# Performance work log

Hardware: AMD Instinct MI355X
Metric: run time of the kernel (lower is better)

## Reference

```python
import jax, jax.numpy as jnp
import numpy as np

DIM = 192; HEADS = 6; HDIM = DIM // HEADS
WS = (2, 8, 8); SS = (1, 4, 4)
B, D, H, W = 2, 8, 64, 64
N = WS[0] * WS[1] * WS[2]          # 128 tokens per window
MLP_H = int(DIM * 2.0)
SCALE = HDIM ** -0.5


def _rel_pos_index_np():
    wd, wh, ww = WS
    coords = np.stack(np.meshgrid(np.arange(wd), np.arange(wh), np.arange(ww), indexing='ij'))
    cf = coords.reshape(3, -1)                      # (3, N)
    rel = (cf[:, :, None] - cf[:, None, :]).transpose(1, 2, 0)  # (N, N, 3)
    rel[..., 0] += wd - 1; rel[..., 1] += wh - 1; rel[..., 2] += ww - 1
    rel[..., 0] *= (2 * wh - 1) * (2 * ww - 1)
    rel[..., 1] *= (2 * ww - 1)
    return rel.sum(-1).astype(np.int32)            # (N, N)


def _compute_mask_np():
    wd, wh, ww = WS; sd, sh, sw = SS
    Dp = -(-D // wd) * wd; Hp = -(-H // wh) * wh; Wp = -(-W // ww) * ww
    img = np.zeros((1, Dp, Hp, Wp, 1), np.float32)
    cnt = 0
    for ds in (slice(0, -wd), slice(-wd, -sd), slice(-sd, None)):
        for hs in (slice(0, -wh), slice(-wh, -sh), slice(-sh, None)):
            for vs in (slice(0, -ww), slice(-ww, -sw), slice(-sw, None)):
                img[:, ds, hs, vs, :] = cnt; cnt += 1
    m = img.reshape(1, Dp // wd, wd, Hp // wh, wh, Wp // ww, ww, 1)
    m = m.transpose(0, 1, 3, 5, 2, 4, 6, 7).reshape(-1, N)       # (nW, N)
    am = m[:, None, :] - m[:, :, None]
    return np.where(am != 0, -100.0, 0.0).astype(np.float32)     # (nW, N, N)


def setup_inputs() -> dict:
    key = jax.random.key(0)
    ks = jax.random.split(key, 6)
    f = lambda k, s: (jax.random.normal(k, s, jnp.float32) * 0.02)
    n_bias = (2 * WS[0] - 1) * (2 * WS[1] - 1) * (2 * WS[2] - 1)  # 675
    return dict(
        x=jax.random.normal(ks[0], (B, D, H, W, DIM), jnp.float32),
        mask_matrix=jnp.asarray(_compute_mask_np()),
        rel_pos_index=jnp.asarray(_rel_pos_index_np()),
        gamma1=jnp.ones((DIM,), jnp.float32), beta1=jnp.zeros((DIM,), jnp.float32),
        w_qkv=f(ks[1], (3 * DIM, DIM)), b_qkv=jnp.zeros((3 * DIM,), jnp.float32),
        rpb=f(ks[2], (n_bias, HEADS)),
        w_proj=f(ks[3], (DIM, DIM)), b_proj=jnp.zeros((DIM,), jnp.float32),
        gamma2=jnp.ones((DIM,), jnp.float32), beta2=jnp.zeros((DIM,), jnp.float32),
        w_fc1=f(ks[4], (MLP_H, DIM)), b_fc1=jnp.zeros((MLP_H,), jnp.float32),
        w_fc2=f(ks[5], (DIM, MLP_H)), b_fc2=jnp.zeros((DIM,), jnp.float32),
    )


def _ln(x, g, b, eps=1e-5):
    mu = x.mean(-1, keepdims=True)
    var = ((x - mu) ** 2).mean(-1, keepdims=True)
    return (x - mu) * jax.lax.rsqrt(var + eps) * g + b


def _stl(x, mask, rpi, gamma1, beta1, w_qkv, b_qkv, rpb, w_proj, b_proj,
         gamma2, beta2, w_fc1, b_fc1, w_fc2, b_fc2):
    wd, wh, ww = WS; sd, sh, sw = SS
    # ---- part1: LN -> pad -> roll -> window attention -> reverse ----
    xn = _ln(x, gamma1, beta1)
    pd = (wd - D % wd) % wd; ph = (wh - H % wh) % wh; pw = (ww - W % ww) % ww
    xn = jnp.pad(xn, ((0, 0), (0, pd), (0, ph), (0, pw), (0, 0)))
    Dp, Hp, Wp = D + pd, H + ph, W + pw
    sx = jnp.roll(xn, (-sd, -sh, -sw), axis=(1, 2, 3))
    # window partition -> (Bw, N, C)
    xw = sx.reshape(B, Dp // wd, wd, Hp // wh, wh, Wp // ww, ww, DIM)
    xw = xw.transpose(0, 1, 3, 5, 2, 4, 6, 7).reshape(-1, N, DIM)
    Bw = xw.shape[0]
    qkv = (xw @ w_qkv.T + b_qkv).reshape(Bw, N, 3, HEADS, HDIM).transpose(2, 0, 3, 1, 4)
    q, k, v = qkv[0] * SCALE, qkv[1], qkv[2]
    attn = jnp.einsum('bhnd,bhmd->bhnm', q, k)
    bias = rpb[rpi.reshape(-1)].reshape(N, N, HEADS).transpose(2, 0, 1)  # (H, N, N)
    attn = attn + bias[None]
    nW = mask.shape[0]
    attn = (attn.reshape(Bw // nW, nW, HEADS, N, N) + mask[None, :, None]).reshape(Bw, HEADS, N, N)
    attn = jax.nn.softmax(attn, axis=-1)
    out = jnp.einsum('bhnm,bhmd->bhnd', attn, v).transpose(0, 2, 1, 3).reshape(Bw, N, DIM)
    out = out @ w_proj.T + b_proj
    # window reverse -> un-roll -> slice
    sx = out.reshape(B, Dp // wd, Hp // wh, Wp // ww, wd, wh, ww, DIM)
    sx = sx.transpose(0, 1, 4, 2, 5, 3, 6, 7).reshape(B, Dp, Hp, Wp, DIM)
    part1 = jnp.roll(sx, (sd, sh, sw), axis=(1, 2, 3))[:, :D, :H, :W, :]
    x = x + part1
    # ---- part2: LN -> MLP (GELU, exact) ----
    y = _ln(x, gamma2, beta2)
    h = jax.nn.gelu(y @ w_fc1.T + b_fc1, approximate=False)
    return x + (h @ w_fc2.T + b_fc2)


def reference(x, mask_matrix, rel_pos_index, gamma1, beta1, w_qkv, b_qkv, rpb,
              w_proj, b_proj, gamma2, beta2, w_fc1, b_fc1, w_fc2, b_fc2):
    return _stl(x, mask_matrix, rel_pos_index, gamma1, beta1, w_qkv, b_qkv, rpb,
                w_proj, b_proj, gamma2, beta2, w_fc1, b_fc1, w_fc2, b_fc2)
```

## Files before the change

kernel.cpp:

```cpp
#include <hip/hip_runtime.h>
#include <hip/hip_bf16.h>
#include <math.h>

#define TOKS   65536
#define DIMC   192
#define NTOK   128
#define MLPH   384
#define QSCALE 0.17677669529663687f

typedef unsigned short u16;
typedef unsigned int   u32;
typedef __attribute__((ext_vector_type(8))) short bf16x8;
typedef __attribute__((ext_vector_type(4))) float f32x4;

static __device__ __forceinline__ float gelu_exact(float v) {
    return 0.5f * v * (1.f + erff(v * 0.70710678118654752f));
}
static __device__ __forceinline__ u16 f2bf(float f) {
    __hip_bfloat16 h = __float2bfloat16(f);
    return *reinterpret_cast<u16*>(&h);
}
static __device__ __forceinline__ float bf2f(u16 b) {
    u32 u = ((u32)b) << 16;
    float f;
    __builtin_memcpy(&f, &u, 4);
    return f;
}
static __device__ __forceinline__ void gl_lds16(const u16* g, u16* l) {
    __builtin_amdgcn_global_load_lds(
        (const __attribute__((address_space(1))) void*)g,
        (__attribute__((address_space(3))) void*)l, 16, 0, 0);
}

#define OFF_XW   0u
#define OFF_Q    6291456u
#define OFF_K    12582912u
#define OFF_V    18874368u
#define OFF_BF   25165824u
#define OFF_WB   25264128u

__global__ __launch_bounds__(256) void k_cvt(const float* __restrict__ a,
                                             const float* __restrict__ b,
                                             const float* __restrict__ c,
                                             const float* __restrict__ d,
                                             u16* __restrict__ o) {
    int i = blockIdx.x * 256 + threadIdx.x;
    float v;
    if (i < 110592) v = a[i];
    else if (i < 147456) v = b[i - 110592];
    else if (i < 221184) v = c[i - 147456];
    else v = d[i - 221184];
    o[i] = f2bf(v);
}

__global__ __launch_bounds__(256) void k_bias(const float* __restrict__ rpb,
                                              const int* __restrict__ rpi,
                                              u16* __restrict__ biasw) {
    int idx = blockIdx.x * 256 + threadIdx.x;
    int h = idx >> 14;
    int n = (idx >> 7) & 127;
    int slot = idx & 127;
    int m = ((slot & 7) << 4) + (slot >> 3);
    biasw[idx] = f2bf(rpb[rpi[n * 128 + m] * 6 + h]);
}

template<bool PERMUTE>
__global__ __launch_bounds__(256) void k_ln(const float* __restrict__ x,
                                            const float* __restrict__ gamma,
                                            const float* __restrict__ beta,
                                            u16* __restrict__ out) {
    int tid  = threadIdx.x;
    int lane = tid & 63, wv = tid >> 6;
    int tk = blockIdx.x * 4 + wv;
    size_t src;
    if (PERMUTE) {
        int w_all = tk >> 7, t = tk & 127;
        int b  = w_all >> 8, rem = w_all & 255;
        int di = rem >> 6, hi = (rem >> 3) & 7, wi = rem & 7;
        int qd = (di * 2 + (t >> 6) + 1) & 7;
        int qh = (hi * 8 + ((t >> 3) & 7) + 4) & 63;
        int qw = (wi * 8 + (t & 7) + 4) & 63;
        src = ((size_t)(((b * 8 + qd) * 64 + qh) * 64 + qw)) * DIMC;
    } else {
        src = (size_t)tk * DIMC;
    }
    float v0 = x[src + lane];
    float v1 = x[src + 64 + lane];
    float v2 = x[src + 128 + lane];
    float s  = v0 + v1 + v2;
    float sq = v0 * v0 + v1 * v1 + v2 * v2;
    #pragma unroll
    for (int off = 32; off; off >>= 1) {
        s  += __shfl_xor(s, off);
        sq += __shfl_xor(sq, off);
    }
    float mu   = s * (1.f / 192.f);
    float var  = sq * (1.f / 192.f) - mu * mu;
    float rstd = rsqrtf(var + 1e-5f);
    size_t o = (size_t)tk * DIMC;
    out[o + lane]       = f2bf((v0 - mu) * rstd * gamma[lane]       + beta[lane]);
    out[o + 64 + lane]  = f2bf((v1 - mu) * rstd * gamma[64 + lane]  + beta[64 + lane]);
    out[o + 128 + lane] = f2bf((v2 - mu) * rstd * gamma[128 + lane] + beta[128 + lane]);
}

template<int MODE, int KD>
__global__ __launch_bounds__(256) void k_mgemm(const u16* __restrict__ A,
                                               const u16* __restrict__ W,
                                               const float* __restrict__ bias,
                                               void* __restrict__ outp,
                                               const float* __restrict__ aux,
                                               u16* __restrict__ q_o,
                                               u16* __restrict__ k_o,
                                               u16* __restrict__ v_o) {
    __shared__ u16 As[2][128 * 64];
    u16*   Eu = (u16*)As;
    float* Ef = (float*)As;
    const int tid = threadIdx.x;
    const int wv = tid >> 6, l = tid & 63;
    const int l15 = l & 15, g4 = l >> 4;
    const int wm = wv >> 1, wn = wv & 1;
    const size_t m0 = (size_t)blockIdx.x * 128;
    const int n0 = blockIdx.y * 64;
    const int srow = l >> 3, scol = l & 7;

    f32x4 acc[4][2] = {};

    auto STAGE = [&](int b, int t) {
        const u16* Ab = A + m0 * KD + t * 64;
        #pragma unroll
        for (int j = 0; j < 4; ++j) {
            int row = (wv * 4 + j) * 8 + srow;
            int sc  = scol ^ (row & 7);
            gl_lds16(Ab + (size_t)row * KD + sc * 8, &As[b][(wv * 4 + j) * 512]);
        }
    };
    auto COMPUTE = [&](int b, int t) {
        #pragma unroll
        for (int kk = 0; kk < 2; ++kk) {
            bf16x8 bfr[2];
            #pragma unroll
            for (int nt = 0; nt < 2; ++nt)
                bfr[nt] = *(const bf16x8*)&W[(size_t)(n0 + wn * 32 + nt * 16 + l15) * KD
                                             + t * 64 + kk * 32 + g4 * 8];
            #pragma unroll
            for (int mt = 0; mt < 4; ++mt) {
                int row  = wm * 64 + mt * 16 + l15;
                int slot = (kk * 4 + g4) ^ (row & 7);
                bf16x8 afr = *(const bf16x8*)&As[b][row * 64 + slot * 8];
                #pragma unroll
                for (int nt = 0; nt < 2; ++nt)
                    acc[mt][nt] = __builtin_amdgcn_mfma_f32_16x16x32_bf16(afr, bfr[nt],
                                                                          acc[mt][nt], 0, 0, 0);
            }
        }
    };

    constexpr int NT = KD / 64;
    STAGE(0, 0);
    __syncthreads();
    for (int t = 0; t < NT; ++t) {
        if (t + 1 < NT) STAGE((t + 1) & 1, t + 1);
        COMPUTE(t & 1, t);
        __syncthreads();
    }

    const int w = (int)(m0 >> 7);

    if (MODE == 0 || MODE == 2) {
        const int sel = (MODE == 0) ? ((n0 >= 384) ? 2 : (n0 >= 192 ? 1 : 0)) : 0;
        const float scl = (MODE == 0 && sel == 0) ? QSCALE : 1.f;
        #pragma unroll
        for (int mt = 0; mt < 4; ++mt) {
            #pragma unroll
            for (int nt = 0; nt < 2; ++nt) {
                int c = wn * 32 + nt * 16 + l15;
                float bb = bias[n0 + c];
                #pragma unroll
                for (int reg = 0; reg < 4; ++reg) {
                    int r = wm * 64 + mt * 16 + g4 * 4 + reg;
                    float v = acc[mt][nt][reg] + bb;
                    if (MODE == 2) v = gelu_exact(v);
                    else v *= scl;
                    int slot8 = (c >> 3) ^ ((r >> 2) & 7);
                    Eu[r * 64 + slot8 * 8 + (c & 7)] = f2bf(v);
                }
            }
        }
        __syncthreads();
        if (MODE == 2) {
            u16* out = (u16*)outp;
            #pragma unroll
            for (int p = 0; p < 4; ++p) {
                int cid = p * 256 + tid;
                int r = cid >> 3, j = cid & 7;
                int slot8 = j ^ ((r >> 2) & 7);
                bf16x8 vv = *(const bf16x8*)&Eu[r * 64 + slot8 * 8];
                *(bf16x8*)&out[(m0 + r) * MLPH + n0 + j * 8] = vv;
            }
        } else if (sel < 2) {
            u16* dst = sel ? k_o : q_o;
            const int hbase = (n0 - sel * 192) >> 5;
            #pragma unroll
            for (int p = 0; p < 4; ++p) {
                int cid = p * 256 + tid;
                int r = cid >> 3, j = cid & 7;
                int c0 = j * 8;
                int slot8 = j ^ ((r >> 2) & 7);
                bf16x8 vv = *(const bf16x8*)&Eu[r * 64 + slot8 * 8];
                size_t b9 = (size_t)(w * 6 + hbase + (c0 >> 5)) * 4096;
                *(bf16x8*)&dst[b9 + (size_t)r * 32 + (c0 & 31)] = vv;
            }
        } else {
            const int hbase = (n0 - 384) >> 5;
            #pragma unroll
            for (int p = 0; p < 4; ++p) {
                int cid = p * 256 + tid;
                int c = cid >> 4, jt = cid & 15;
                int t0 = jt * 8;
                u16 tmp[8];
                #pragma unroll
                for (int i = 0; i < 8; ++i) {
                    int r = t0 + i;
                    int slot8 = (c >> 3) ^ ((r >> 2) & 7);
                    tmp[i] = Eu[r * 64 + slot8 * 8 + (c & 7)];
                }
                size_t b9 = (size_t)(w * 6 + hbase + (c >> 5)) * 4096;
                *(bf16x8*)&v_o[b9 + (size_t)(c & 31) * 128 + t0] = *(bf16x8*)tmp;
            }
        }
    } else {
        #pragma unroll
        for (int mt = 0; mt < 4; ++mt) {
            #pragma unroll
            for (int nt = 0; nt < 2; ++nt) {
                int c = wn * 32 + nt * 16 + l15;
                float bb = bias[n0 + c];
                #pragma unroll
                for (int reg = 0; reg < 4; ++reg) {
                    int r = wm * 64 + mt * 16 + g4 * 4 + reg;
                    int swz = (c >> 2) ^ ((r >> 2) & 3);
                    Ef[r * 64 + swz * 4 + (c & 3)] = acc[mt][nt][reg] + bb;
                }
            }
        }
        __syncthreads();
        float* out = (float*)outp;
        #pragma unroll
        for (int p = 0; p < 8; ++p) {
            int cid = p * 256 + tid;
            int r = cid >> 4, j = cid & 15;
            int swz = j ^ ((r >> 2) & 3);
            float4 vv = *(const float4*)&Ef[r * 64 + swz * 4];
            size_t drow;
            if (MODE == 1) {
                int m = (int)m0 + r;
                int w_all = m >> 7, tt = m & 127;
                int b  = w_all >> 8, rem = w_all & 255;
                int di = rem >> 6, hi = (rem >> 3) & 7, wi = rem & 7;
                int qd = (di * 2 + (tt >> 6) + 1) & 7;
                int qh = (hi * 8 + ((tt >> 3) & 7) + 4) & 63;
                int qw = (wi * 8 + (tt & 7) + 4) & 63;
                drow = (size_t)(((b * 8 + qd) * 64 + qh) * 64 + qw) * DIMC;
            } else {
                drow = (m0 + r) * DIMC;
            }
            float4 ax = *(const float4*)&aux[drow + n0 + j * 4];
            vv.x += ax.x; vv.y += ax.y; vv.z += ax.z; vv.w += ax.w;
            *(float4*)&out[drow + n0 + j * 4] = vv;
        }
    }
}

__global__ __launch_bounds__(256) void k_attn(const u16* __restrict__ qb,
                                              const u16* __restrict__ kb,
                                              const u16* __restrict__ vb,
                                              const u16* __restrict__ biasw,
                                              u16* __restrict__ attn_out) {
    __shared__ u16 Pl[4][32 * 128];
    u16* Ou = (u16*)Pl;
    int wh = blockIdx.x;
    int w_all = wh / 6, head = wh - w_all * 6;
    int wl = w_all & 255;
    int tid = threadIdx.x;
    int wv = tid >> 6, l = tid & 63;
    int l15 = l & 15, g4 = l >> 4;
    size_t base = (size_t)wh * 4096;
    const u16* qg = qb + base;
    const u16* kg = kb + base;
    const u16* vg = vb + base;
    int rowb = wv * 32;

    bf16x8 qa[2];
    #pragma unroll
    for (int rt = 0; rt < 2; ++rt)
        qa[rt] = *(const bf16x8*)&qg[(size_t)(rowb + rt * 16 + l15) * 32 + g4 * 8];

    f32x4 s[2][8] = {};
    #pragma unroll
    for (int ct = 0; ct < 8; ++ct) {
        bf16x8 kf = *(const bf16x8*)&kg[(size_t)(ct * 16 + l15) * 32 + g4 * 8];
        s[0][ct] = __builtin_amdgcn_mfma_f32_16x16x32_bf16(qa[0], kf, s[0][ct], 0, 0, 0);
        s[1][ct] = __builtin_amdgcn_mfma_f32_16x16x32_bf16(qa[1], kf, s[1][ct], 0, 0, 0);
    }

    int di = wl >> 6, hi = (wl >> 3) & 7, wi = wl & 7;
    auto rcode = [&](int t) {
        int d = di * 2 + (t >> 6);
        int h = hi * 8 + ((t >> 3) & 7);
        int w = wi * 8 + (t & 7);
        int rd = (d < 6) ? 0 : (d < 7 ? 1 : 2);
        int rh = (h < 56) ? 0 : (h < 60 ? 1 : 2);
        int rw = (w < 56) ? 0 : (w < 60 ? 1 : 2);
        return rd * 9 + rh * 3 + rw;
    };
    int rm[8];
    #pragma unroll
    for (int ct = 0; ct < 8; ++ct) rm[ct] = rcode(ct * 16 + l15);

    const u16* bh = biasw + (size_t)head * 16384;
    #pragma unroll
    for (int rt = 0; rt < 2; ++rt)
        #pragma unroll
        for (int reg = 0; reg < 4; ++reg) {
            int n = rowb + rt * 16 + g4 * 4 + reg;
            int rn = rcode(n);
            bf16x8 bv = *(const bf16x8*)&bh[(size_t)n * 128 + l15 * 8];
            #pragma unroll
            for (int ct = 0; ct < 8; ++ct) {
                float mval = (rn == rm[ct]) ? 0.f : -100.f;
                s[rt][ct][reg] += bf2f((u16)bv[ct]) + mval;
            }
        }

    u16* Pw = Pl[wv];
    #pragma unroll
    for (int rt = 0; rt < 2; ++rt)
        #pragma unroll
        for (int reg = 0; reg < 4; ++reg) {
            float mx = -1e30f;
            #pragma unroll
            for (int ct = 0; ct < 8; ++ct) mx = fmaxf(mx, s[rt][ct][reg]);
            #pragma unroll
            for (int off = 1; off < 16; off <<= 1) mx = fmaxf(mx, __shfl_xor(mx, off));
            float sum = 0.f;
            #pragma unroll
            for (int ct = 0; ct < 8; ++ct) {
                float p = __expf(s[rt][ct][reg] - mx);
                s[rt][ct][reg] = p; sum += p;
            }
            #pragma unroll
            for (int off = 1; off < 16; off <<= 1) sum += __shfl_xor(sum, off);
            float inv = 1.f / sum;
            int nloc = rt * 16 + g4 * 4 + reg;
            int sw = ((nloc >> 2) & 3) << 4;
            #pragma unroll
            for (int ct = 0; ct < 8; ++ct) {
                int m = ct * 16 + l15;
                Pw[nloc * 128 + (m ^ sw)] = f2bf(s[rt][ct][reg] * inv);
            }
        }
    __syncthreads();

    f32x4 o[2][2] = {};
    #pragma unroll
    for (int kt = 0; kt < 4; ++kt) {
        bf16x8 vf[2];
        #pragma unroll
        for (int dt = 0; dt < 2; ++dt)
            vf[dt] = *(const bf16x8*)&vg[(size_t)(dt * 16 + l15) * 128 + kt * 32 + g4 * 8];
        #pragma unroll
        for (int rt = 0; rt < 2; ++rt) {
            int nloc = rt * 16 + l15;
            int sw = ((nloc >> 2) & 3) << 4;
            int m8 = kt * 32 + g4 * 8;
            bf16x8 pa = *(const bf16x8*)&Pw[nloc * 128 + (m8 ^ sw)];
            #pragma unroll
            for (int dt = 0; dt < 2; ++dt)
                o[rt][dt] = __builtin_amdgcn_mfma_f32_16x16x32_bf16(pa, vf[dt], o[rt][dt], 0, 0, 0);
        }
    }

    __syncthreads();
    #pragma unroll
    for (int rt = 0; rt < 2; ++rt)
        #pragma unroll
        for (int dt = 0; dt < 2; ++dt)
            #pragma unroll
            for (int reg = 0; reg < 4; ++reg) {
                int r = rowb + rt * 16 + g4 * 4 + reg;
                int c = dt * 16 + l15;
                int slot8 = (c >> 3) ^ ((r >> 2) & 3);
                Ou[r * 32 + slot8 * 8 + (c & 7)] = f2bf(o[rt][dt][reg]);
            }
    __syncthreads();
    #pragma unroll
    for (int p = 0; p < 2; ++p) {
        int cid = p * 256 + tid;
        int r = cid >> 2, j = cid & 3;
        int slot8 = j ^ ((r >> 2) & 3);
        bf16x8 vv = *(const bf16x8*)&Ou[r * 32 + slot8 * 8];
        *(bf16x8*)&attn_out[((size_t)(w_all * 128 + r)) * DIMC + head * 32 + j * 8] = vv;
    }
}

extern "C" void kernel_launch(void* const* d_in, const int* in_sizes, int n_in,
                              void* d_out, int out_size, void* d_ws, size_t ws_size,
                              hipStream_t stream) {
    const float* x      = (const float*)d_in[0];
    const int*   rpi    = (const int*)d_in[2];
    const float* gamma1 = (const float*)d_in[3];
    const float* beta1  = (const float*)d_in[4];
    const float* w_qkv  = (const float*)d_in[5];
    const float* b_qkv  = (const float*)d_in[6];
    const float* rpb    = (const float*)d_in[7];
    const float* w_proj = (const float*)d_in[8];
    const float* b_proj = (const float*)d_in[9];
    const float* gamma2 = (const float*)d_in[10];
    const float* beta2  = (const float*)d_in[11];
    const float* w_fc1  = (const float*)d_in[12];
    const float* b_fc1  = (const float*)d_in[13];
    const float* w_fc2  = (const float*)d_in[14];
    const float* b_fc2  = (const float*)d_in[15];

    float* ws    = (float*)d_ws;
    u16*   xwu   = (u16*)(ws + OFF_XW);
    u16*   qbu   = (u16*)(ws + OFF_Q);
    u16*   kbu   = (u16*)(ws + OFF_K);
    u16*   vbu   = (u16*)(ws + OFF_V);
    u16*   hbu   = (u16*)(ws + OFF_Q);
    u16*   ybu   = (u16*)(ws + OFF_V);
    u16*   biasw = (u16*)(ws + OFF_BF);
    u16*   wb    = (u16*)(ws + OFF_WB);
    float* xres  = (float*)d_out;

    const u16* wqkv_b  = wb;
    const u16* wproj_b = wb + 110592;
    const u16* wfc1_b  = wb + 147456;
    const u16* wfc2_b  = wb + 221184;

    k_cvt<<<1152, 256, 0, stream>>>(w_qkv, w_proj, w_fc1, w_fc2, wb);
    k_bias<<<384, 256, 0, stream>>>(rpb, rpi, biasw);
    k_ln<true><<<16384, 256, 0, stream>>>(x, gamma1, beta1, xwu);
    k_mgemm<0, 192><<<dim3(512, 9), 256, 0, stream>>>(xwu, wqkv_b, b_qkv, nullptr, nullptr,
                                                      qbu, kbu, vbu);
    k_attn<<<3072, 256, 0, stream>>>(qbu, kbu, vbu, biasw, xwu);
    k_mgemm<1, 192><<<dim3(512, 3), 256, 0, stream>>>(xwu, wproj_b, b_proj, xres, x,
                                                      nullptr, nullptr, nullptr);
    k_ln<false><<<16384, 256, 0, stream>>>(xres, gamma2, beta2, ybu);
    k_mgemm<2, 192><<<dim3(512, 6), 256, 0, stream>>>(ybu, wfc1_b, b_fc1, hbu, nullptr,
                                                      nullptr, nullptr, nullptr);
    k_mgemm<3, 384><<<dim3(512, 3), 256, 0, stream>>>(hbu, wfc2_b, b_fc2, xres, xres,
                                                      nullptr, nullptr, nullptr);
}
```

Baseline: 216.7 us.

## Retile GEMMs to 64x192 blocks staging full K slab once

The four GEMM kernels are replaced by one that computes a 64-row by 192-column output tile per block. It loads a whole 192-wide K slab of A into LDS at once, so A is read once per 192 output columns rather than once per 64. Weight fragments are still read straight from global memory, and the epilogue loops over three 64-column chunks through LDS. This removes redundant A traffic and per-K-step barriers, at the cost of losing double-buffered overlap and using more accumulator registers, which may lower occupancy.

```diff
diff --git a/kernel.cpp b/kernel.cpp
--- a/kernel.cpp
+++ b/kernel.cpp
@@ -103,170 +103,181 @@
     out[o + 128 + lane] = f2bf((v2 - mu) * rstd * gamma[128 + lane] + beta[128 + lane]);
 }
 
-template<int MODE, int KD>
-__global__ __launch_bounds__(256) void k_mgemm(const u16* __restrict__ A,
-                                               const u16* __restrict__ W,
-                                               const float* __restrict__ bias,
-                                               void* __restrict__ outp,
-                                               const float* __restrict__ aux,
-                                               u16* __restrict__ q_o,
-                                               u16* __restrict__ k_o,
-                                               u16* __restrict__ v_o) {
-    __shared__ u16 As[2][128 * 64];
-    u16*   Eu = (u16*)As;
+template<int MODE>
+__global__ __launch_bounds__(256) void k_gA(const u16* __restrict__ A,
+                                            const u16* __restrict__ W,
+                                            const float* __restrict__ bias,
+                                            void* __restrict__ outp,
+                                            const float* __restrict__ aux,
+                                            u16* __restrict__ q_o,
+                                            u16* __restrict__ k_o,
+                                            u16* __restrict__ v_o) {
+    constexpr int KD = (MODE == 3) ? 384 : 192;
+    __shared__ u16 As[3 * 64 * 64];
+    u16*   Eu = As;
     float* Ef = (float*)As;
     const int tid = threadIdx.x;
     const int wv = tid >> 6, l = tid & 63;
     const int l15 = l & 15, g4 = l >> 4;
     const int wm = wv >> 1, wn = wv & 1;
-    const size_t m0 = (size_t)blockIdx.x * 128;
-    const int n0 = blockIdx.y * 64;
-    const int srow = l >> 3, scol = l & 7;
-
-    f32x4 acc[4][2] = {};
-
-    auto STAGE = [&](int b, int t) {
-        const u16* Ab = A + m0 * KD + t * 64;
-        #pragma unroll
-        for (int j = 0; j < 4; ++j) {
-            int row = (wv * 4 + j) * 8 + srow;
-            int sc  = scol ^ (row & 7);
-            gl_lds16(Ab + (size_t)row * KD + sc * 8, &As[b][(wv * 4 + j) * 512]);
+    const size_t m0 = (size_t)blockIdx.x * 64;
+    const int sel = (MODE == 0) ? blockIdx.y : 0;
+    const int nb0 = (MODE == 0) ? sel * 192 : (MODE == 2) ? blockIdx.y * 192 : 0;
+    const int w  = (int)(m0 >> 7);
+    const int hh = (int)(m0 >> 6) & 1;
+
+    f32x4 acc[3][2][2] = {};
+
+    auto STAGEP = [&](int p) {
+        const u16* Ab = A + m0 * KD + p * 192;
+        #pragma unroll
+        for (int j = 0; j < 6; ++j) {
+            int cid = j * 256 + tid;
+            int tile = cid >> 9, r = (cid >> 3) & 63, sl = cid & 7;
+            int sc = sl ^ (r & 7);
+            gl_lds16(Ab + (size_t)r * KD + tile * 64 + sc * 8,
+                     &As[(size_t)(j * 256 + wv * 64) * 8]);
         }
     };
-    auto COMPUTE = [&](int b, int t) {
-        #pragma unroll
-        for (int kk = 0; kk < 2; ++kk) {
-            bf16x8 bfr[2];
-            #pragma unroll
-            for (int nt = 0; nt < 2; ++nt)
-                bfr[nt] = *(const bf16x8*)&W[(size_t)(n0 + wn * 32 + nt * 16 + l15) * KD
-                                             + t * 64 + kk * 32 + g4 * 8];
-            #pragma unroll
-            for (int mt = 0; mt < 4; ++mt) {
-                int row  = wm * 64 + mt * 16 + l15;
-                int slot = (kk * 4 + g4) ^ (row & 7);
-                bf16x8 afr = *(const bf16x8*)&As[b][row * 64 + slot * 8];
+    auto KLOOP = [&](int kbase) {
+        #pragma unroll
+        for (int kt = 0; kt < 6; ++kt) {
+            int kglob = kbase + kt;
+            bf16x8 bfr[3][2];
+            #pragma unroll
+            for (int j = 0; j < 3; ++j)
                 #pragma unroll
                 for (int nt = 0; nt < 2; ++nt)
-                    acc[mt][nt] = __builtin_amdgcn_mfma_f32_16x16x32_bf16(afr, bfr[nt],
-                                                                          acc[mt][nt], 0, 0, 0);
+                    bfr[j][nt] = *(const bf16x8*)&W[(size_t)(nb0 + j * 64 + wn * 32 + nt * 16 + l15) * KD
+                                                   + kglob * 32 + g4 * 8];
+            #pragma unroll
+            for (int mt = 0; mt < 2; ++mt) {
+                int row  = wm * 32 + mt * 16 + l15;
+                int slot = ((kt & 1) * 4 + g4) ^ (row & 7);
+                bf16x8 afr = *(const bf16x8*)&As[(size_t)((kt >> 1) * 64 + row) * 64 + slot * 8];
+                #pragma unroll
+                for (int j = 0; j < 3; ++j)
+                    #pragma unroll
+                    for (int nt = 0; nt < 2; ++nt)
+                        acc[j][mt][nt] = __builtin_amdgcn_mfma_f32_16x16x32_bf16(afr, bfr[j][nt],
+                                                                                 acc[j][mt][nt], 0, 0, 0);
             }
         }
     };
 
-    constexpr int NT = KD / 64;
-    STAGE(0, 0);
+    STAGEP(0);
     __syncthreads();
-    for (int t = 0; t < NT; ++t) {
-        if (t + 1 < NT) STAGE((t + 1) & 1, t + 1);
-        COMPUTE(t & 1, t);
+    KLOOP(0);
+    if (MODE == 3) {
         __syncthreads();
-    }
-
-    const int w = (int)(m0 >> 7);
-
-    if (MODE == 0 || MODE == 2) {
-        const int sel = (MODE == 0) ? ((n0 >= 384) ? 2 : (n0 >= 192 ? 1 : 0)) : 0;
-        const float scl = (MODE == 0 && sel == 0) ? QSCALE : 1.f;
-        #pragma unroll
-        for (int mt = 0; mt < 4; ++mt) {
-            #pragma unroll
-            for (int nt = 0; nt < 2; ++nt) {
-                int c = wn * 32 + nt * 16 + l15;
-                float bb = bias[n0 + c];
-                #pragma unroll
-                for (int reg = 0; reg < 4; ++reg) {
-                    int r = wm * 64 + mt * 16 + g4 * 4 + reg;
-                    float v = acc[mt][nt][reg] + bb;
-                    if (MODE == 2) v = gelu_exact(v);
-                    else v *= scl;
-                    int slot8 = (c >> 3) ^ ((r >> 2) & 7);
-                    Eu[r * 64 + slot8 * 8 + (c & 7)] = f2bf(v);
-                }
-            }
-        }
+        STAGEP(1);
         __syncthreads();
-        if (MODE == 2) {
-            u16* out = (u16*)outp;
+        KLOOP(6);
+    }
+    __syncthreads();
+
+    #pragma unroll
+    for (int j = 0; j < 3; ++j) {
+        const int nb = nb0 + j * 64;
+        if (MODE == 0 || MODE == 2) {
+            const float scl = (MODE == 0 && sel == 0) ? QSCALE : 1.f;
+            #pragma unroll
+            for (int mt = 0; mt < 2; ++mt)
+                #pragma unroll
+                for (int nt = 0; nt < 2; ++nt) {
+                    int c = wn * 32 + nt * 16 + l15;
+                    float bb = bias[nb + c];
+                    #pragma unroll
+                    for (int reg = 0; reg < 4; ++reg) {
+                        int r = wm * 32 + mt * 16 + g4 * 4 + reg;
+                        float v = acc[j][mt][nt][reg] + bb;
+                        if (MODE == 2) v = gelu_exact(v);
+                        else v *= scl;
+                        int slot8 = (c >> 3) ^ ((r >> 2) & 7);
+                        Eu[r * 64 + slot8 * 8 + (c & 7)] = f2bf(v);
+                    }
+                }
+            __syncthreads();
+            if (MODE == 2) {
+                u16* out = (u16*)outp;
+                #pragma unroll
+                for (int p = 0; p < 2; ++p) {
+                    int cid = p * 256 + tid;
+                    int r = cid >> 3, jj = cid & 7;
+                    int slot8 = jj ^ ((r >> 2) & 7);
+                    bf16x8 vv = *(const bf16x8*)&Eu[r * 64 + slot8 * 8];
+                    *(bf16x8*)&out[(m0 + r) * MLPH + nb + jj * 8] = vv;
+                }
+            } else if (sel < 2) {
+                u16* dst = sel ? k_o : q_o;
+                #pragma unroll
+                for (int p = 0; p < 2; ++p) {
+                    int cid = p * 256 + tid;
+                    int r = cid >> 3, jj = cid & 7;
+                    int c0 = jj * 8;
+                    int slot8 = jj ^ ((r >> 2) & 7);
+                    bf16x8 vv = *(const bf16x8*)&Eu[r * 64 + slot8 * 8];
+                    size_t b9 = (size_t)(w * 6 + j * 2 + (c0 >> 5)) * 4096;
+                    *(bf16x8*)&dst[b9 + (size_t)(hh * 64 + r) * 32 + (c0 & 31)] = vv;
+                }
+            } else {
+                #pragma unroll
+                for (int p = 0; p < 2; ++p) {
+                    int cid = p * 256 + tid;
+                    int c = cid >> 3, jt = cid & 7;
+                    int t0 = jt * 8;
+                    u16 tmp[8];
+                    #pragma unroll
+                    for (int i = 0; i < 8; ++i) {
+                        int r = t0 + i;
+                        int slot8 = (c >> 3) ^ ((r >> 2) & 7);
+                        tmp[i] = Eu[r * 64 + slot8 * 8 + (c & 7)];
+                    }
+                    size_t b9 = (size_t)(w * 6 + j * 2 + (c >> 5)) * 4096;
+                    *(bf16x8*)&v_o[b9 + (size_t)(c & 31) * 128 + hh * 64 + t0] = *(bf16x8*)tmp;
+                }
+            }
+            __syncthreads();
+        } else {
+            #pragma unroll
+            for (int mt = 0; mt < 2; ++mt)
+                #pragma unroll
+                for (int nt = 0; nt < 2; ++nt) {
+                    int c = wn * 32 + nt * 16 + l15;
+                    float bb = bias[nb + c];
+                    #pragma unroll
+                    for (int reg = 0; reg < 4; ++reg) {
+                        int r = wm * 32 + mt * 16 + g4 * 4 + reg;
+                        int swz = (c >> 2) ^ ((r >> 2) & 3);
+                        Ef[r * 64 + swz * 4 + (c & 3)] = acc[j][mt][nt][reg] + bb;
+                    }
+                }
+            __syncthreads();
+            float* out = (float*)outp;
             #pragma unroll
             for (int p = 0; p < 4; ++p) {
                 int cid = p * 256 + tid;
-                int r = cid >> 3, j = cid & 7;
-                int slot8 = j ^ ((r >> 2) & 7);
-                bf16x8 vv = *(const bf16x8*)&Eu[r * 64 + slot8 * 8];
-                *(bf16x8*)&out[(m0 + r) * MLPH + n0 + j * 8] = vv;
-            }
-        } else if (sel < 2) {
-            u16* dst = sel ? k_o : q_o;
-            const int hbase = (n0 - sel * 192) >> 5;
-            #pragma unroll
-            for (int p = 0; p < 4; ++p) {
-                int cid = p * 256 + tid;
-                int r = cid >> 3, j = cid & 7;
-                int c0 = j * 8;
-                int slot8 = j ^ ((r >> 2) & 7);
-                bf16x8 vv = *(const bf16x8*)&Eu[r * 64 + slot8 * 8];
-                size_t b9 = (size_t)(w * 6 + hbase + (c0 >> 5)) * 4096;
-                *(bf16x8*)&dst[b9 + (size_t)r * 32 + (c0 & 31)] = vv;
-            }
-        } else {
-            const int hbase = (n0 - 384) >> 5;
-            #pragma unroll
-            for (int p = 0; p < 4; ++p) {
-                int cid = p * 256 + tid;
-                int c = cid >> 4, jt = cid & 15;
-                int t0 = jt * 8;
-                u16 tmp[8];
-                #pragma unroll
-                for (int i = 0; i < 8; ++i) {
-                    int r = t0 + i;
-                    int slot8 = (c >> 3) ^ ((r >> 2) & 7);
-                    tmp[i] = Eu[r * 64 + slot8 * 8 + (c & 7)];
-                }
-                size_t b9 = (size_t)(w * 6 + hbase + (c >> 5)) * 4096;
-                *(bf16x8*)&v_o[b9 + (size_t)(c & 31) * 128 + t0] = *(bf16x8*)tmp;
-            }
-        }
-    } else {
-        #pragma unroll
-        for (int mt = 0; mt < 4; ++mt) {
-            #pragma unroll
-            for (int nt = 0; nt < 2; ++nt) {
-                int c = wn * 32 + nt * 16 + l15;
-                float bb = bias[n0 + c];
-                #pragma unroll
-                for (int reg = 0; reg < 4; ++reg) {
-                    int r = wm * 64 + mt * 16 + g4 * 4 + reg;
-                    int swz = (c >> 2) ^ ((r >> 2) & 3);
-                    Ef[r * 64 + swz * 4 + (c & 3)] = acc[mt][nt][reg] + bb;
-                }
-            }
-        }
-        __syncthreads();
-        float* out = (float*)outp;
-        #pragma unroll
-        for (int p = 0; p < 8; ++p) {
-            int cid = p * 256 + tid;
-            int r = cid >> 4, j = cid & 15;
-            int swz = j ^ ((r >> 2) & 3);
-            float4 vv = *(const float4*)&Ef[r * 64 + swz * 4];
-            size_t drow;
-            if (MODE == 1) {
-                int m = (int)m0 + r;
-                int w_all = m >> 7, tt = m & 127;
-                int b  = w_all >> 8, rem = w_all & 255;
-                int di = rem >> 6, hi = (rem >> 3) & 7, wi = rem & 7;
-                int qd = (di * 2 + (tt >> 6) + 1) & 7;
-                int qh = (hi * 8 + ((tt >> 3) & 7) + 4) & 63;
-                int qw = (wi * 8 + (tt & 7) + 4) & 63;
-                drow = (size_t)(((b * 8 + qd) * 64 + qh) * 64 + qw) * DIMC;
-            } else {
-                drow = (m0 + r) * DIMC;
-            }
-            float4 ax = *(const float4*)&aux[drow + n0 + j * 4];
-            vv.x += ax.x; vv.y += ax.y; vv.z += ax.z; vv.w += ax.w;
-            *(float4*)&out[drow + n0 + j * 4] = vv;
+                int r = cid >> 4, jj = cid & 15;
+                int swz = jj ^ ((r >> 2) & 3);
+                float4 vv = *(const float4*)&Ef[r * 64 + swz * 4];
+                size_t drow;
+                if (MODE == 1) {
+                    int m = (int)m0 + r;
+                    int w_all = m >> 7, tt = m & 127;
+                    int b  = w_all >> 8, rem = w_all & 255;
+                    int di = rem >> 6, hi = (rem >> 3) & 7, wi = rem & 7;
+                    int qd = (di * 2 + (tt >> 6) + 1) & 7;
+                    int qh = (hi * 8 + ((tt >> 3) & 7) + 4) & 63;
+                    int qw = (wi * 8 + (tt & 7) + 4) & 63;
+                    drow = (size_t)(((b * 8 + qd) * 64 + qh) * 64 + qw) * DIMC;
+                } else {
+                    drow = (m0 + r) * DIMC;
+                }
+                float4 ax = *(const float4*)&aux[drow + nb + jj * 4];
+                vv.x += ax.x; vv.y += ax.y; vv.z += ax.z; vv.w += ax.w;
+                *(float4*)&out[drow + nb + jj * 4] = vv;
+            }
+            __syncthreads();
         }
     }
 }
@@ -441,14 +452,14 @@
     k_cvt<<<1152, 256, 0, stream>>>(w_qkv, w_proj, w_fc1, w_fc2, wb);
     k_bias<<<384, 256, 0, stream>>>(rpb, rpi, biasw);
     k_ln<true><<<16384, 256, 0, stream>>>(x, gamma1, beta1, xwu);
-    k_mgemm<0, 192><<<dim3(512, 9), 256, 0, stream>>>(xwu, wqkv_b, b_qkv, nullptr, nullptr,
-                                                      qbu, kbu, vbu);
+    k_gA<0><<<dim3(1024, 3), 256, 0, stream>>>(xwu, wqkv_b, b_qkv, nullptr, nullptr,
+                                               qbu, kbu, vbu);
     k_attn<<<3072, 256, 0, stream>>>(qbu, kbu, vbu, biasw, xwu);
-    k_mgemm<1, 192><<<dim3(512, 3), 256, 0, stream>>>(xwu, wproj_b, b_proj, xres, x,
-                                                      nullptr, nullptr, nullptr);
+    k_gA<1><<<1024, 256, 0, stream>>>(xwu, wproj_b, b_proj, xres, x,
+                                      nullptr, nullptr, nullptr);
     k_ln<false><<<16384, 256, 0, stream>>>(xres, gamma2, beta2, ybu);
-    k_mgemm<2, 192><<<dim3(512, 6), 256, 0, stream>>>(ybu, wfc1_b, b_fc1, hbu, nullptr,
-                                                      nullptr, nullptr, nullptr);
-    k_mgemm<3, 384><<<dim3(512, 3), 256, 0, stream>>>(hbu, wfc2_b, b_fc2, xres, xres,
-                                                      nullptr, nullptr, nullptr);
-}
+    k_gA<2><<<dim3(1024, 2), 256, 0, stream>>>(ybu, wfc1_b, b_fc1, hbu, nullptr,
+                                               nullptr, nullptr, nullptr);
+    k_gA<3><<<1024, 256, 0, stream>>>(hbu, wfc2_b, b_fc2, xres, xres,
+                                      nullptr, nullptr, nullptr);
+}
```

After: 276.9 us. 27.8% more time.

## Widen GEMM N-tiles to reuse A across sub-tiles and merge prep kernels

Applied to the files above, without the earlier changes.

The GEMM kernel now computes NSUB 64-column sub-tiles per block, so each A tile is staged into LDS once and reused across up to 192 output columns. This cuts the repeated A reads that the old 9/6/3-way column grids caused. The K loop now stages three 64-wide A slices up front instead of double-buffering, which removes the load/compute overlap and triples LDS use. Register pressure also rises with 24 accumulators, and the grids shrink to as few as 512 blocks. The weight-conversion and bias-gather kernels are merged into one launch.

```diff
diff --git a/kernel.cpp b/kernel.cpp
--- a/kernel.cpp
+++ b/kernel.cpp
@@ -39,29 +39,31 @@
 #define OFF_BF   25165824u
 #define OFF_WB   25264128u
 
-__global__ __launch_bounds__(256) void k_cvt(const float* __restrict__ a,
-                                             const float* __restrict__ b,
-                                             const float* __restrict__ c,
-                                             const float* __restrict__ d,
-                                             u16* __restrict__ o) {
-    int i = blockIdx.x * 256 + threadIdx.x;
-    float v;
-    if (i < 110592) v = a[i];
-    else if (i < 147456) v = b[i - 110592];
-    else if (i < 221184) v = c[i - 147456];
-    else v = d[i - 221184];
-    o[i] = f2bf(v);
-}
-
-__global__ __launch_bounds__(256) void k_bias(const float* __restrict__ rpb,
+__global__ __launch_bounds__(256) void k_prep(const float* __restrict__ a,
+                                              const float* __restrict__ b,
+                                              const float* __restrict__ c,
+                                              const float* __restrict__ d,
+                                              u16* __restrict__ o,
+                                              const float* __restrict__ rpb,
                                               const int* __restrict__ rpi,
                                               u16* __restrict__ biasw) {
-    int idx = blockIdx.x * 256 + threadIdx.x;
-    int h = idx >> 14;
-    int n = (idx >> 7) & 127;
-    int slot = idx & 127;
-    int m = ((slot & 7) << 4) + (slot >> 3);
-    biasw[idx] = f2bf(rpb[rpi[n * 128 + m] * 6 + h]);
+    int bid = blockIdx.x;
+    if (bid < 1152) {
+        int i = bid * 256 + threadIdx.x;
+        float v;
+        if (i < 110592) v = a[i];
+        else if (i < 147456) v = b[i - 110592];
+        else if (i < 221184) v = c[i - 147456];
+        else v = d[i - 221184];
+        o[i] = f2bf(v);
+    } else {
+        int idx = (bid - 1152) * 256 + threadIdx.x;
+        int h = idx >> 14;
+        int n = (idx >> 7) & 127;
+        int slot = idx & 127;
+        int m = ((slot & 7) << 4) + (slot >> 3);
+        biasw[idx] = f2bf(rpb[rpi[n * 128 + m] * 6 + h]);
+    }
 }
 
 template<bool PERMUTE>
@@ -103,7 +105,7 @@
     out[o + 128 + lane] = f2bf((v2 - mu) * rstd * gamma[128 + lane] + beta[128 + lane]);
 }
 
-template<int MODE, int KD>
+template<int MODE, int KD, int NSUB>
 __global__ __launch_bounds__(256) void k_mgemm(const u16* __restrict__ A,
                                                const u16* __restrict__ W,
                                                const float* __restrict__ bias,
@@ -112,7 +114,7 @@
                                                u16* __restrict__ q_o,
                                                u16* __restrict__ k_o,
                                                u16* __restrict__ v_o) {
-    __shared__ u16 As[2][128 * 64];
+    __shared__ u16 As[3][128 * 64];
     u16*   Eu = (u16*)As;
     float* Ef = (float*)As;
     const int tid = threadIdx.x;
@@ -120,13 +122,15 @@
     const int l15 = l & 15, g4 = l >> 4;
     const int wm = wv >> 1, wn = wv & 1;
     const size_t m0 = (size_t)blockIdx.x * 128;
-    const int n0 = blockIdx.y * 64;
+    const int nb0 = blockIdx.y * (NSUB * 64);
+    const int sel = (MODE == 0) ? blockIdx.y : 0;
     const int srow = l >> 3, scol = l & 7;
-
-    f32x4 acc[4][2] = {};
-
-    auto STAGE = [&](int b, int t) {
-        const u16* Ab = A + m0 * KD + t * 64;
+    const int w = (int)(m0 >> 7);
+
+    f32x4 acc[NSUB][4][2] = {};
+
+    auto STAGE = [&](int b, int tcol) {
+        const u16* Ab = A + m0 * KD + tcol * 64;
         #pragma unroll
         for (int j = 0; j < 4; ++j) {
             int row = (wv * 4 + j) * 8 + srow;
@@ -134,139 +138,147 @@
             gl_lds16(Ab + (size_t)row * KD + sc * 8, &As[b][(wv * 4 + j) * 512]);
         }
     };
-    auto COMPUTE = [&](int b, int t) {
+    auto COMPUTE = [&](int b, int tglob) {
         #pragma unroll
         for (int kk = 0; kk < 2; ++kk) {
-            bf16x8 bfr[2];
-            #pragma unroll
-            for (int nt = 0; nt < 2; ++nt)
-                bfr[nt] = *(const bf16x8*)&W[(size_t)(n0 + wn * 32 + nt * 16 + l15) * KD
-                                             + t * 64 + kk * 32 + g4 * 8];
+            bf16x8 bfr[NSUB][2];
+            #pragma unroll
+            for (int j = 0; j < NSUB; ++j)
+                #pragma unroll
+                for (int nt = 0; nt < 2; ++nt)
+                    bfr[j][nt] = *(const bf16x8*)&W[(size_t)(nb0 + j * 64 + wn * 32 + nt * 16 + l15) * KD
+                                                   + tglob * 64 + kk * 32 + g4 * 8];
             #pragma unroll
             for (int mt = 0; mt < 4; ++mt) {
                 int row  = wm * 64 + mt * 16 + l15;
                 int slot = (kk * 4 + g4) ^ (row & 7);
                 bf16x8 afr = *(const bf16x8*)&As[b][row * 64 + slot * 8];
                 #pragma unroll
-                for (int nt = 0; nt < 2; ++nt)
-                    acc[mt][nt] = __builtin_amdgcn_mfma_f32_16x16x32_bf16(afr, bfr[nt],
-                                                                          acc[mt][nt], 0, 0, 0);
+                for (int j = 0; j < NSUB; ++j)
+                    #pragma unroll
+                    for (int nt = 0; nt < 2; ++nt)
+                        acc[j][mt][nt] = __builtin_amdgcn_mfma_f32_16x16x32_bf16(afr, bfr[j][nt],
+                                                                                 acc[j][mt][nt], 0, 0, 0);
             }
         }
     };
 
-    constexpr int NT = KD / 64;
-    STAGE(0, 0);
+    constexpr int NPH = KD / 192;
+    #pragma unroll
+    for (int ph = 0; ph < NPH; ++ph) {
+        if (ph) __syncthreads();
+        STAGE(0, ph * 3 + 0);
+        STAGE(1, ph * 3 + 1);
+        STAGE(2, ph * 3 + 2);
+        __syncthreads();
+        COMPUTE(0, ph * 3 + 0);
+        COMPUTE(1, ph * 3 + 1);
+        COMPUTE(2, ph * 3 + 2);
+    }
     __syncthreads();
-    for (int t = 0; t < NT; ++t) {
-        if (t + 1 < NT) STAGE((t + 1) & 1, t + 1);
-        COMPUTE(t & 1, t);
-        __syncthreads();
-    }
-
-    const int w = (int)(m0 >> 7);
-
-    if (MODE == 0 || MODE == 2) {
-        const int sel = (MODE == 0) ? ((n0 >= 384) ? 2 : (n0 >= 192 ? 1 : 0)) : 0;
-        const float scl = (MODE == 0 && sel == 0) ? QSCALE : 1.f;
-        #pragma unroll
-        for (int mt = 0; mt < 4; ++mt) {
-            #pragma unroll
-            for (int nt = 0; nt < 2; ++nt) {
-                int c = wn * 32 + nt * 16 + l15;
-                float bb = bias[n0 + c];
-                #pragma unroll
-                for (int reg = 0; reg < 4; ++reg) {
-                    int r = wm * 64 + mt * 16 + g4 * 4 + reg;
-                    float v = acc[mt][nt][reg] + bb;
-                    if (MODE == 2) v = gelu_exact(v);
-                    else v *= scl;
-                    int slot8 = (c >> 3) ^ ((r >> 2) & 7);
-                    Eu[r * 64 + slot8 * 8 + (c & 7)] = f2bf(v);
-                }
-            }
-        }
-        __syncthreads();
-        if (MODE == 2) {
-            u16* out = (u16*)outp;
-            #pragma unroll
-            for (int p = 0; p < 4; ++p) {
+
+    #pragma unroll
+    for (int j = 0; j < NSUB; ++j) {
+        const int nb = nb0 + j * 64;
+        if (MODE == 0 || MODE == 2) {
+            const float scl = (MODE == 0 && sel == 0) ? QSCALE : 1.f;
+            #pragma unroll
+            for (int mt = 0; mt < 4; ++mt)
+                #pragma unroll
+                for (int nt = 0; nt < 2; ++nt) {
+                    int c = wn * 32 + nt * 16 + l15;
+                    float bb = bias[nb + c];
+                    #pragma unroll
+                    for (int reg = 0; reg < 4; ++reg) {
+                        int r = wm * 64 + mt * 16 + g4 * 4 + reg;
+                        float v = acc[j][mt][nt][reg] + bb;
+                        if (MODE == 2) v = gelu_exact(v);
+                        else v *= scl;
+                        int slot8 = (c >> 3) ^ ((r >> 2) & 7);
+                        Eu[r * 64 + slot8 * 8 + (c & 7)] = f2bf(v);
+                    }
+                }
+            __syncthreads();
+            if (MODE == 2) {
+                u16* out = (u16*)outp;
+                #pragma unroll
+                for (int p = 0; p < 4; ++p) {
+                    int cid = p * 256 + tid;
+                    int r = cid >> 3, jj = cid & 7;
+                    int slot8 = jj ^ ((r >> 2) & 7);
+                    bf16x8 vv = *(const bf16x8*)&Eu[r * 64 + slot8 * 8];
+                    *(bf16x8*)&out[(m0 + r) * MLPH + nb + jj * 8] = vv;
+                }
+            } else if (sel < 2) {
+                u16* dst = sel ? k_o : q_o;
+                #pragma unroll
+                for (int p = 0; p < 4; ++p) {
+                    int cid = p * 256 + tid;
+                    int r = cid >> 3, jj = cid & 7;
+                    int c0 = jj * 8;
+                    int slot8 = jj ^ ((r >> 2) & 7);
+                    bf16x8 vv = *(const bf16x8*)&Eu[r * 64 + slot8 * 8];
+                    size_t b9 = (size_t)(w * 6 + j * 2 + (c0 >> 5)) * 4096;
+                    *(bf16x8*)&dst[b9 + (size_t)r * 32 + (c0 & 31)] = vv;
+                }
+            } else {
+                #pragma unroll
+                for (int p = 0; p < 4; ++p) {
+                    int cid = p * 256 + tid;
+                    int c = cid >> 4, jt = cid & 15;
+                    int t0 = jt * 8;
+                    u16 tmp[8];
+                    #pragma unroll
+                    for (int i = 0; i < 8; ++i) {
+                        int r = t0 + i;
+                        int slot8 = (c >> 3) ^ ((r >> 2) & 7);
+                        tmp[i] = Eu[r * 64 + slot8 * 8 + (c & 7)];
+                    }
+                    size_t b9 = (size_t)(w * 6 + j * 2 + (c >> 5)) * 4096;
+                    *(bf16x8*)&v_o[b9 + (size_t)(c & 31) * 128 + t0] = *(bf16x8*)tmp;
+                }
+            }
+            __syncthreads();
+        } else {
+            #pragma unroll
+            for (int mt = 0; mt < 4; ++mt)
+                #pragma unroll
+                for (int nt = 0; nt < 2; ++nt) {
+                    int c = wn * 32 + nt * 16 + l15;
+                    float bb = bias[nb + c];
+                    #pragma unroll
+                    for (int reg = 0; reg < 4; ++reg) {
+                        int r = wm * 64 + mt * 16 + g4 * 4 + reg;
+                        int swz = (c >> 2) ^ ((r >> 2) & 3);
+                        Ef[r * 64 + swz * 4 + (c & 3)] = acc[j][mt][nt][reg] + bb;
+                    }
+                }
+            __syncthreads();
+            float* out = (float*)outp;
+            #pragma unroll
+            for (int p = 0; p < 8; ++p) {
                 int cid = p * 256 + tid;
-                int r = cid >> 3, j = cid & 7;
-                int slot8 = j ^ ((r >> 2) & 7);
-                bf16x8 vv = *(const bf16x8*)&Eu[r * 64 + slot8 * 8];
-                *(bf16x8*)&out[(m0 + r) * MLPH + n0 + j * 8] = vv;
-            }
-        } else if (sel < 2) {
-            u16* dst = sel ? k_o : q_o;
-            const int hbase = (n0 - sel * 192) >> 5;
-            #pragma unroll
-            for (int p = 0; p < 4; ++p) {
-                int cid = p * 256 + tid;
-                int r = cid >> 3, j = cid & 7;
-                int c0 = j * 8;
-                int slot8 = j ^ ((r >> 2) & 7);
-                bf16x8 vv = *(const bf16x8*)&Eu[r * 64 + slot8 * 8];
-                size_t b9 = (size_t)(w * 6 + hbase + (c0 >> 5)) * 4096;
-                *(bf16x8*)&dst[b9 + (size_t)r * 32 + (c0 & 31)] = vv;
-            }
-        } else {
-            const int hbase = (n0 - 384) >> 5;
-            #pragma unroll
-            for (int p = 0; p < 4; ++p) {
-                int cid = p * 256 + tid;
-                int c = cid >> 4, jt = cid & 15;
-                int t0 = jt * 8;
-                u16 tmp[8];
-                #pragma unroll
-                for (int i = 0; i < 8; ++i) {
-                    int r = t0 + i;
-                    int slot8 = (c >> 3) ^ ((r >> 2) & 7);
-                    tmp[i] = Eu[r * 64 + slot8 * 8 + (c & 7)];
-                }
-                size_t b9 = (size_t)(w * 6 + hbase + (c >> 5)) * 4096;
-                *(bf16x8*)&v_o[b9 + (size_t)(c & 31) * 128 + t0] = *(bf16x8*)tmp;
-            }
-        }
-    } else {
-        #pragma unroll
-        for (int mt = 0; mt < 4; ++mt) {
-            #pragma unroll
-            for (int nt = 0; nt < 2; ++nt) {
-                int c = wn * 32 + nt * 16 + l15;
-                float bb = bias[n0 + c];
-                #pragma unroll
-                for (int reg = 0; reg < 4; ++reg) {
-                    int r = wm * 64 + mt * 16 + g4 * 4 + reg;
-                    int swz = (c >> 2) ^ ((r >> 2) & 3);
-                    Ef[r * 64 + swz * 4 + (c & 3)] = acc[mt][nt][reg] + bb;
-                }
-            }
-        }
-        __syncthreads();
-        float* out = (float*)outp;
-        #pragma unroll
-        for (int p = 0; p < 8; ++p) {
-            int cid = p * 256 + tid;
-            int r = cid >> 4, j = cid & 15;
-            int swz = j ^ ((r >> 2) & 3);
-            float4 vv = *(const float4*)&Ef[r * 64 + swz * 4];
-            size_t drow;
-            if (MODE == 1) {
-                int m = (int)m0 + r;
-                int w_all = m >> 7, tt = m & 127;
-                int b  = w_all >> 8, rem = w_all & 255;
-                int di = rem >> 6, hi = (rem >> 3) & 7, wi = rem & 7;
-                int qd = (di * 2 + (tt >> 6) + 1) & 7;
-                int qh = (hi * 8 + ((tt >> 3) & 7) + 4) & 63;
-                int qw = (wi * 8 + (tt & 7) + 4) & 63;
-                drow = (size_t)(((b * 8 + qd) * 64 + qh) * 64 + qw) * DIMC;
-            } else {
-                drow = (m0 + r) * DIMC;
-            }
-            float4 ax = *(const float4*)&aux[drow + n0 + j * 4];
-            vv.x += ax.x; vv.y += ax.y; vv.z += ax.z; vv.w += ax.w;
-            *(float4*)&out[drow + n0 + j * 4] = vv;
+                int r = cid >> 4, jj = cid & 15;
+                int swz = jj ^ ((r >> 2) & 3);
+                float4 vv = *(const float4*)&Ef[r * 64 + swz * 4];
+                size_t drow;
+                if (MODE == 1) {
+                    int m = (int)m0 + r;
+                    int w_all = m >> 7, tt = m & 127;
+                    int b  = w_all >> 8, rem = w_all & 255;
+                    int di = rem >> 6, hi = (rem >> 3) & 7, wi = rem & 7;
+                    int qd = (di * 2 + (tt >> 6) + 1) & 7;
+                    int qh = (hi * 8 + ((tt >> 3) & 7) + 4) & 63;
+                    int qw = (wi * 8 + (tt & 7) + 4) & 63;
+                    drow = (size_t)(((b * 8 + qd) * 64 + qh) * 64 + qw) * DIMC;
+                } else {
+                    drow = (m0 + r) * DIMC;
+                }
+                float4 ax = *(const float4*)&aux[drow + nb + jj * 4];
+                vv.x += ax.x; vv.y += ax.y; vv.z += ax.z; vv.w += ax.w;
+                *(float4*)&out[drow + nb + jj * 4] = vv;
+            }
+            __syncthreads();
         }
     }
 }
@@ -438,17 +450,16 @@
     const u16* wfc1_b  = wb + 147456;
     const u16* wfc2_b  = wb + 221184;
 
-    k_cvt<<<1152, 256, 0, stream>>>(w_qkv, w_proj, w_fc1, w_fc2, wb);
-    k_bias<<<384, 256, 0, stream>>>(rpb, rpi, biasw);
+    k_prep<<<1536, 256, 0, stream>>>(w_qkv, w_proj, w_fc1, w_fc2, wb, rpb, rpi, biasw);
     k_ln<true><<<16384, 256, 0, stream>>>(x, gamma1, beta1, xwu);
-    k_mgemm<0, 192><<<dim3(512, 9), 256, 0, stream>>>(xwu, wqkv_b, b_qkv, nullptr, nullptr,
-                                                      qbu, kbu, vbu);
+    k_mgemm<0, 192, 3><<<dim3(512, 3), 256, 0, stream>>>(xwu, wqkv_b, b_qkv, nullptr, nullptr,
+                                                         qbu, kbu, vbu);
     k_attn<<<3072, 256, 0, stream>>>(qbu, kbu, vbu, biasw, xwu);
-    k_mgemm<1, 192><<<dim3(512, 3), 256, 0, stream>>>(xwu, wproj_b, b_proj, xres, x,
-                                                      nullptr, nullptr, nullptr);
+    k_mgemm<1, 192, 1><<<dim3(512, 3), 256, 0, stream>>>(xwu, wproj_b, b_proj, xres, x,
+                                                         nullptr, nullptr, nullptr);
     k_ln<false><<<16384, 256, 0, stream>>>(xres, gamma2, beta2, ybu);
-    k_mgemm<2, 192><<<dim3(512, 6), 256, 0, stream>>>(ybu, wfc1_b, b_fc1, hbu, nullptr,
-                                                      nullptr, nullptr, nullptr);
-    k_mgemm<3, 384><<<dim3(512, 3), 256, 0, stream>>>(hbu, wfc2_b, b_fc2, xres, xres,
-                                                      nullptr, nullptr, nullptr);
-}
+    k_mgemm<2, 192, 3><<<dim3(512, 2), 256, 0, stream>>>(ybu, wfc1_b, b_fc1, hbu, nullptr,
+                                                         nullptr, nullptr, nullptr);
+    k_mgemm<3, 384, 3><<<dim3(512, 1), 256, 0, stream>>>(hbu, wfc2_b, b_fc2, xres, xres,
+                                                         nullptr, nullptr, nullptr);
+}
```

Measured after the change: 242.6 us. +12.0%, slower.
